# Kernel tuning notes

Measured on AMD Instinct MI355X. Metric: run time of the kernel, lower is better.

## Reference

```python
import jax, jax.numpy as jnp
import numpy as np
from jax import lax

# Problem constants (mirroring scalar_born args / init_kwargs)
NY = NX = 400          # interior model size
NS = 4                 # shots
NSRC = 1               # sources per shot
NREC = 100             # receivers per shot
NT = 300               # time steps
CHUNK = 10             # inner scan length (NT % CHUNK == 0)
PML = 20               # pml_width
FD_PAD = 2             # accuracy // 2 for accuracy=4
PAD = PML + FD_PAD
DX = 5.0               # grid_spacing
DT = 5e-4              # dt
PML_FREQ = 25.0
VMAX = 2500.0          # max_vel used for PML profile

# 4th-order central FD coefficients (taps at offsets -2..+2)
C1 = (1.0 / 12, -2.0 / 3, 0.0, 2.0 / 3, -1.0 / 12)        # d/dx, * 1/h
C2 = (-1.0 / 12, 4.0 / 3, -5.0 / 2, 4.0 / 3, -1.0 / 12)   # d2/dx2, * 1/h^2


def _deriv(w, coefs, axis, scale):
    """4th-order central difference along `axis` with zero boundary."""
    pad = [(0, 0)] * w.ndim
    pad[axis] = (2, 2)
    p = jnp.pad(w, pad)
    n = w.shape[axis]
    out = coefs[0] * lax.slice_in_dim(p, 0, n, axis=axis)
    for k in range(1, 5):
        if coefs[k] != 0.0:
            out = out + coefs[k] * lax.slice_in_dim(p, k, k + n, axis=axis)
    return out * scale


def _pml_profiles(n):
    """CPML decay (a) and update (b) 1D profiles over a padded axis."""
    i = jnp.arange(n, dtype=jnp.float32)
    frac = jnp.maximum(jnp.clip((PAD - i) / PML, 0.0, 1.0),
                       jnp.clip((i - (n - 1 - PAD)) / PML, 0.0, 1.0))
    L = PML * DX
    sigma_max = 3.0 * VMAX * np.log(1000.0) / (2.0 * L)
    sigma = sigma_max * frac ** 2
    alpha = np.pi * PML_FREQ
    a = jnp.exp(-(sigma + alpha) * DT)
    b = jnp.where(sigma > 0, sigma / (sigma + alpha) * (a - 1.0), 0.0)
    return a, b


def _propagate(v, scatter, source_amplitudes, source_locations,
               receiver_locations, bg_receiver_locations):
    v_pad = jnp.pad(v, PAD, mode='edge')     # 'replicate' pad for velocity
    sc_pad = jnp.pad(scatter, PAD)           # 'constant' (zero) pad for scatter
    npy, npx = v_pad.shape
    ay, by = _pml_profiles(npy)
    ax, bx = _pml_profiles(npx)
    ay, by = ay[:, None], by[:, None]
    ax, bx = ax[None, :], bx[None, :]
    v2dt2 = (v_pad * DT) ** 2
    born_scale = 2.0 * v_pad * sc_pad * DT * DT  # Born secondary-source scale

    sy = source_locations[..., 0] + PAD          # [ns, nsrc]
    sx = source_locations[..., 1] + PAD
    shot_s = jnp.arange(NS)[:, None]
    v_src = v_pad[sy, sx]
    sc_src = sc_pad[sy, sx]
    # Source scaling as in scalar_born(): bg gets -f*v^2*dt^2,
    # scattered gets -2*f*v*scatter*dt^2 at the source cell.
    f_bg = -source_amplitudes * (v_src ** 2)[..., None] * DT * DT
    f_sc = -2.0 * source_amplitudes * (v_src * sc_src)[..., None] * DT * DT
    f_bg = jnp.moveaxis(f_bg, -1, 0).reshape(NT // CHUNK, CHUNK, NS, NSRC)
    f_sc = jnp.moveaxis(f_sc, -1, 0).reshape(NT // CHUNK, CHUNK, NS, NSRC)

    ry = receiver_locations[..., 0] + PAD
    rx = receiver_locations[..., 1] + PAD
    rby = bg_receiver_locations[..., 0] + PAD
    rbx = bg_receiver_locations[..., 1] + PAD
    shot_r = jnp.arange(NS)[:, None]

    inv_h, inv_h2 = 1.0 / DX, 1.0 / (DX * DX)

    def pml_lap(w, psiy, psix, zetay, zetax):
        # CPML (Pasalic & McGarry) memory variables for 2nd-order scalar wave eq
        dwdy = _deriv(w, C1, -2, inv_h)
        dwdx = _deriv(w, C1, -1, inv_h)
        d2y = _deriv(w, C2, -2, inv_h2)
        d2x = _deriv(w, C2, -1, inv_h2)
        psiy = ay * psiy + by * dwdy
        psix = ax * psix + bx * dwdx
        dpsiy = _deriv(psiy, C1, -2, inv_h)
        dpsix = _deriv(psix, C1, -1, inv_h)
        zetay = ay * zetay + by * (d2y + dpsiy)
        zetax = ax * zetax + bx * (d2x + dpsix)
        lap = d2y + d2x + dpsiy + dpsix + zetay + zetax
        return lap, psiy, psix, zetay, zetax

    def step(carry, fs):
        (wfc, wfp, psiy, psix, zetay, zetax,
         wfcsc, wfpsc, psiysc, psixsc, zetaysc, zetaxsc) = carry
        fb, fsc = fs
        lap, psiy, psix, zetay, zetax = pml_lap(wfc, psiy, psix, zetay, zetax)
        wfn = v2dt2 * lap + 2.0 * wfc - wfp
        wfn = wfn.at[shot_s, sy, sx].add(fb)
        lapsc, psiysc, psixsc, zetaysc, zetaxsc = pml_lap(
            wfcsc, psiysc, psixsc, zetaysc, zetaxsc)
        wfnsc = v2dt2 * lapsc + 2.0 * wfcsc - wfpsc + born_scale * lap
        wfnsc = wfnsc.at[shot_s, sy, sx].add(fsc)
        rec_bg = wfn[shot_r, rby, rbx]
        rec_sc = wfnsc[shot_r, ry, rx]
        new_carry = (wfn, wfc, psiy, psix, zetay, zetax,
                     wfnsc, wfcsc, psiysc, psixsc, zetaysc, zetaxsc)
        return new_carry, (rec_bg, rec_sc)

    chunk = jax.checkpoint(lambda c, xs: lax.scan(step, c, xs))

    z = jnp.zeros((NS, npy, npx), dtype=v.dtype)
    carry0 = (z,) * 12
    carry, (rec_bg, rec_sc) = lax.scan(chunk, carry0, (f_bg, f_sc))
    rec_bg = jnp.moveaxis(rec_bg.reshape(NT, NS, NREC), 0, -1)
    rec_sc = jnp.moveaxis(rec_sc.reshape(NT, NS, NREC), 0, -1)
    return carry, rec_bg, rec_sc


def setup_inputs() -> dict:
    key = jax.random.key(0)
    k = jax.random.split(key, 6)
    v = 1500.0 + 1000.0 * jax.random.uniform(k[0], (NY, NX), jnp.float32)
    scatter = 0.1 * jax.random.normal(k[1], (NY, NX), jnp.float32)
    source_amplitudes = jax.random.normal(k[2], (NS, NSRC, NT), jnp.float32)
    source_locations = jax.random.randint(k[3], (NS, NSRC, 2), 0, NY)
    receiver_locations = jax.random.randint(k[4], (NS, NREC, 2), 0, NY)
    bg_receiver_locations = jax.random.randint(k[5], (NS, NREC, 2), 0, NY)
    return {
        'v': v,
        'scatter': scatter,
        'source_amplitudes': source_amplitudes,
        'source_locations': source_locations,
        'receiver_locations': receiver_locations,
        'bg_receiver_locations': bg_receiver_locations,
    }


def reference(v, scatter, source_amplitudes, source_locations,
              receiver_locations, bg_receiver_locations):
    carry, rec_bg, rec_sc = _propagate(
        v, scatter, source_amplitudes, source_locations,
        receiver_locations, bg_receiver_locations)
    # (final background wavefield, final scattered wavefield,
    #  background receiver amplitudes, scattered receiver amplitudes)
    return (carry[0], carry[6], rec_bg, rec_sc)
```

## Files before the change

### kernel.cpp

```cpp
#include <hip/hip_runtime.h>
#include <hip/hip_bf16.h>


constexpr int NYX  = 400;
constexpr int NS   = 4;
constexpr int NREC = 100;
constexpr int NT   = 300;
constexpr int PAD  = 22;
constexpr int NP   = 444;
constexpr int NP2  = NP * NP;
constexpr int SNP2 = NS * NP2;
constexpr float DT    = 0.0005f;
constexpr float INVH  = 0.2f;
constexpr float INVH2 = 0.04f;
constexpr float C1A = 1.0f / 12.0f;
constexpr float C1B = 2.0f / 3.0f;
constexpr float C2A = -1.0f / 12.0f;
constexpr float C2B = 4.0f / 3.0f;
constexpr float C2C = -2.5f;

__device__ __align__(16) float g_w[2][2 * SNP2];
__device__ __align__(16) float g_px[2][2 * SNP2];
__device__ __align__(16) float g_py[2][2 * SNP2];
__device__ __align__(16) float g_zx[2 * SNP2];
__device__ __align__(16) float g_zy[2 * SNP2];
__device__ __align__(16) float g_vb[2 * NP2];
__device__ float g_pa[NP];
__device__ float g_pb[NP];
__device__ float g_fbg[NT * NS];
__device__ float g_fsc[NT * NS];
__device__ int   g_spos[2 * NS];
__device__ int   g_mode;

__device__ __forceinline__ int clampi(int v, int lo, int hi) {
    return v < lo ? lo : (v > hi ? hi : v);
}
__device__ __forceinline__ float in_ld(const void* p, int i) {
    if (g_mode) return __bfloat162float(((const __hip_bfloat16*)p)[i]);
    return ((const float*)p)[i];
}
__device__ __forceinline__ void out_st(void* p, int i, float v) {
    if (g_mode) ((__hip_bfloat16*)p)[i] = __float2bfloat16(v);
    else        ((float*)p)[i] = v;
}
__device__ __forceinline__ float4 ld4(const float* w, int s, int yy, int i) {
    if ((unsigned)yy >= (unsigned)NP) return make_float4(0.f, 0.f, 0.f, 0.f);
    return *(const float4*)(w + 2 * (s * NP2 + yy * NP + 2 * i));
}

__global__ void detect_mode(const void* vptr) {
    if (threadIdx.x == 0 && blockIdx.x == 0) {
        const __hip_bfloat16* p = (const __hip_bfloat16*)vptr;
        int ok = 1;
        for (int i = 0; i < 32; i += 2) {
            float f = __bfloat162float(p[i]);
            if (!(f >= 1000.f && f <= 3000.f)) ok = 0;
        }
        g_mode = ok;
    }
}

__global__ void zero_state() {
    int i = blockIdx.x * blockDim.x + threadIdx.x;
    if (i >= SNP2 / 2) return;
    float4 z = make_float4(0.f, 0.f, 0.f, 0.f);
    ((float4*)g_w[0])[i] = z;  ((float4*)g_w[1])[i] = z;
    ((float4*)g_px[0])[i] = z; ((float4*)g_px[1])[i] = z;
    ((float4*)g_py[0])[i] = z; ((float4*)g_py[1])[i] = z;
    ((float4*)g_zx)[i] = z;    ((float4*)g_zy)[i] = z;
}

__global__ void prep_pad(const void* __restrict__ v, const void* __restrict__ sc) {
    int i = blockIdx.x * blockDim.x + threadIdx.x;
    if (i >= NP2) return;
    int y = i / NP, x = i % NP;
    int vy = clampi(y - PAD, 0, NYX - 1);
    int vx = clampi(x - PAD, 0, NYX - 1);
    float vv = in_ld(v, vy * NYX + vx);
    float vd = vv * DT;
    float s = 0.f;
    if (y >= PAD && y < PAD + NYX && x >= PAD && x < PAD + NYX)
        s = in_ld(sc, (y - PAD) * NYX + (x - PAD));
    g_vb[2 * i]     = vd * vd;
    g_vb[2 * i + 1] = 2.f * vv * s * DT * DT;
    if (i < NP) {
        float fi = (float)i;
        float f1 = fminf(fmaxf((22.f - fi) * 0.05f, 0.f), 1.f);
        float f2 = fminf(fmaxf((fi - 421.f) * 0.05f, 0.f), 1.f);
        float frac = fmaxf(f1, f2);
        float sigma = 259.0408229f * frac * frac;
        const float alpha = 78.53981634f;
        float a = expf(-(sigma + alpha) * DT);
        g_pa[i] = a;
        g_pb[i] = (sigma > 0.f) ? sigma / (sigma + alpha) * (a - 1.f) : 0.f;
    }
}

__global__ void prep_src(const void* __restrict__ amp, const int* __restrict__ sloc,
                         const void* __restrict__ v, const void* __restrict__ sc) {
    int i = blockIdx.x * blockDim.x + threadIdx.x;
    if (i >= NT * NS) return;
    int s = i % NS, t = i / NS;
    int ly = clampi(sloc[s * 2 + 0], 0, NYX - 1);
    int lx = clampi(sloc[s * 2 + 1], 0, NYX - 1);
    float a  = in_ld(amp, s * NT + t);
    float vv = in_ld(v,  ly * NYX + lx);
    float ss = in_ld(sc, ly * NYX + lx);
    g_fbg[i] = -a * vv * vv * DT * DT;
    g_fsc[i] = -2.f * a * vv * ss * DT * DT;
    if (i < NS) {
        g_spos[2 * i]     = ly + PAD;
        g_spos[2 * i + 1] = lx + PAD;
    }
}

__global__ void __launch_bounds__(256, 7)
step_fused(int t, const int* __restrict__ rloc, const int* __restrict__ rbloc,
           void* __restrict__ out) {
    const int i = threadIdx.x;
    const int bid = blockIdx.x;
    const int s = (bid >> 1) & 3;
    const int y = ((bid & 1) ? 222 : 0) + (bid >> 3);
    const int cur = t & 1, nxt = cur ^ 1;
    __shared__ __align__(16) float sw[904], spx[904];

    if (t > 0 && y == 0 && i < 2 * NREC) {
        int r = i % NREC;
        bool isbg = i < NREC;
        const int* rl = isbg ? rbloc : rloc;
        int ry = clampi(rl[(s * NREC + r) * 2 + 0], 0, NYX - 1) + PAD;
        int rx = clampi(rl[(s * NREC + r) * 2 + 1], 0, NYX - 1) + PAD;
        float val = g_w[cur][2 * (s * NP2 + ry * NP + rx) + (isbg ? 0 : 1)];
        int base = isbg ? (2 * SNP2) : (2 * SNP2 + NS * NREC * NT);
        out_st(out, base + (s * NREC + r) * NT + (t - 1), val);
    }

    const bool active = i < 222;
    const int x0 = 2 * i, x1 = x0 + 1;
    const int yx  = y * NP + x0;
    const int idx = s * NP2 + yx;

    float4 w4 = make_float4(0.f, 0.f, 0.f, 0.f);
    if (active) {
        w4 = *(const float4*)(g_w[cur] + 2 * idx);
        *(float4*)&sw[2 * x0 + 4] = w4;
    } else if (i == 222) {
        #pragma unroll
        for (int k = 0; k < 4; ++k) { sw[k] = 0.f; spx[k] = 0.f; }
    } else if (i == 223) {
        #pragma unroll
        for (int k = 892; k < 904; ++k) { sw[k] = 0.f; spx[k] = 0.f; }
    }
    __syncthreads();

    const bool pxreg = (i <= 11 || i >= 210);
    float pbx0 = 0.f, pbx1 = 0.f, pax0 = 0.f, pax1 = 0.f;
    float d2x_b0 = 0.f, d2x_b1 = 0.f, d2x_s0 = 0.f, d2x_s1 = 0.f;
    float4 pxn = make_float4(0.f, 0.f, 0.f, 0.f);
    float2 tm2, tm1, tp2, tp3;
    if (active) {
        tm2 = *(const float2*)&sw[2 * (x0 - 2) + 4];
        tm1 = *(const float2*)&sw[2 * (x0 - 1) + 4];
        tp2 = *(const float2*)&sw[2 * (x0 + 2) + 4];
        tp3 = *(const float2*)&sw[2 * (x0 + 3) + 4];
        d2x_b0 = (C2A * (tm2.x + tp2.x) + C2B * (tm1.x + w4.z) + C2C * w4.x) * INVH2;
        d2x_s0 = (C2A * (tm2.y + tp2.y) + C2B * (tm1.y + w4.w) + C2C * w4.y) * INVH2;
        d2x_b1 = (C2A * (tm1.x + tp3.x) + C2B * (w4.x + tp2.x) + C2C * w4.z) * INVH2;
        d2x_s1 = (C2A * (tm1.y + tp3.y) + C2B * (w4.y + tp2.y) + C2C * w4.w) * INVH2;
        pbx0 = g_pb[x0]; pbx1 = g_pb[x1];
        pax0 = g_pa[x0]; pax1 = g_pa[x1];
        if (pxreg && pbx0 != 0.f) {
            float4 pxo = *(const float4*)(g_px[cur] + 2 * idx);
            float dwb0 = (C1A * tm2.x - C1B * tm1.x + C1B * w4.z - C1A * tp2.x) * INVH;
            float dws0 = (C1A * tm2.y - C1B * tm1.y + C1B * w4.w - C1A * tp2.y) * INVH;
            float dwb1 = (C1A * tm1.x - C1B * w4.x + C1B * tp2.x - C1A * tp3.x) * INVH;
            float dws1 = (C1A * tm1.y - C1B * w4.y + C1B * tp2.y - C1A * tp3.y) * INVH;
            pxn.x = pax0 * pxo.x + pbx0 * dwb0;
            pxn.y = pax0 * pxo.y + pbx0 * dws0;
            pxn.z = pax1 * pxo.z + pbx1 * dwb1;
            pxn.w = pax1 * pxo.w + pbx1 * dws1;
            *(float4*)(g_px[nxt] + 2 * idx) = pxn;
        }
        *(float4*)&spx[2 * x0 + 4] = pxn;
    }
    __syncthreads();
    if (!active) return;

    float dpx_b0 = 0.f, dpx_b1 = 0.f, dpx_s0 = 0.f, dpx_s1 = 0.f;
    if (pxreg) {
        float2 pm2 = *(const float2*)&spx[2 * (x0 - 2) + 4];
        float2 pm1 = *(const float2*)&spx[2 * (x0 - 1) + 4];
        float2 pp2 = *(const float2*)&spx[2 * (x0 + 2) + 4];
        float2 pp3 = *(const float2*)&spx[2 * (x0 + 3) + 4];
        dpx_b0 = (C1A * pm2.x - C1B * pm1.x + C1B * pxn.z - C1A * pp2.x) * INVH;
        dpx_s0 = (C1A * pm2.y - C1B * pm1.y + C1B * pxn.w - C1A * pp2.y) * INVH;
        dpx_b1 = (C1A * pm1.x - C1B * pxn.x + C1B * pp2.x - C1A * pp3.x) * INVH;
        dpx_s1 = (C1A * pm1.y - C1B * pxn.y + C1B * pp2.y - C1A * pp3.y) * INVH;
    }

    const float pby = g_pb[y];
    const bool yframe = (y <= 23 || y >= 420);
    float d2y_b0, d2y_b1, d2y_s0, d2y_s1;
    float dpy_b0 = 0.f, dpy_b1 = 0.f, dpy_s0 = 0.f, dpy_s1 = 0.f;
    if (yframe) {
        float4 wy[9];
        #pragma unroll
        for (int k = 0; k < 9; ++k)
            wy[k] = (k == 4) ? w4 : ld4(g_w[cur], s, y - 4 + k, i);
        d2y_b0 = (C2A * (wy[2].x + wy[6].x) + C2B * (wy[3].x + wy[5].x) + C2C * wy[4].x) * INVH2;
        d2y_s0 = (C2A * (wy[2].y + wy[6].y) + C2B * (wy[3].y + wy[5].y) + C2C * wy[4].y) * INVH2;
        d2y_b1 = (C2A * (wy[2].z + wy[6].z) + C2B * (wy[3].z + wy[5].z) + C2C * wy[4].z) * INVH2;
        d2y_s1 = (C2A * (wy[2].w + wy[6].w) + C2B * (wy[3].w + wy[5].w) + C2C * wy[4].w) * INVH2;
        float4 pn[5];
        #pragma unroll
        for (int k = 0; k < 5; ++k) {
            int yy = y - 2 + k;
            float pbv = ((unsigned)yy < (unsigned)NP) ? g_pb[yy] : 0.f;
            float4 r = make_float4(0.f, 0.f, 0.f, 0.f);
            if (pbv != 0.f) {
                float pav = g_pa[yy];
                float4 po = *(const float4*)(g_py[cur] + 2 * (s * NP2 + yy * NP + x0));
                float db0 = (C1A * wy[k].x - C1B * wy[k+1].x + C1B * wy[k+3].x - C1A * wy[k+4].x) * INVH;
                float ds0 = (C1A * wy[k].y - C1B * wy[k+1].y + C1B * wy[k+3].y - C1A * wy[k+4].y) * INVH;
                float db1 = (C1A * wy[k].z - C1B * wy[k+1].z + C1B * wy[k+3].z - C1A * wy[k+4].z) * INVH;
                float ds1 = (C1A * wy[k].w - C1B * wy[k+1].w + C1B * wy[k+3].w - C1A * wy[k+4].w) * INVH;
                r.x = pav * po.x + pbv * db0;  r.y = pav * po.y + pbv * ds0;
                r.z = pav * po.z + pbv * db1;  r.w = pav * po.w + pbv * ds1;
            }
            pn[k] = r;
        }
        dpy_b0 = (C1A * pn[0].x - C1B * pn[1].x + C1B * pn[3].x - C1A * pn[4].x) * INVH;
        dpy_s0 = (C1A * pn[0].y - C1B * pn[1].y + C1B * pn[3].y - C1A * pn[4].y) * INVH;
        dpy_b1 = (C1A * pn[0].z - C1B * pn[1].z + C1B * pn[3].z - C1A * pn[4].z) * INVH;
        dpy_s1 = (C1A * pn[0].w - C1B * pn[1].w + C1B * pn[3].w - C1A * pn[4].w) * INVH;
        if (pby != 0.f)
            *(float4*)(g_py[nxt] + 2 * idx) = pn[2];
    } else {
        float4 m2 = *(const float4*)(g_w[cur] + 2 * (idx - 2 * NP));
        float4 m1 = *(const float4*)(g_w[cur] + 2 * (idx - NP));
        float4 p1 = *(const float4*)(g_w[cur] + 2 * (idx + NP));
        float4 p2 = *(const float4*)(g_w[cur] + 2 * (idx + 2 * NP));
        d2y_b0 = (C2A * (m2.x + p2.x) + C2B * (m1.x + p1.x) + C2C * w4.x) * INVH2;
        d2y_s0 = (C2A * (m2.y + p2.y) + C2B * (m1.y + p1.y) + C2C * w4.y) * INVH2;
        d2y_b1 = (C2A * (m2.z + p2.z) + C2B * (m1.z + p1.z) + C2C * w4.z) * INVH2;
        d2y_s1 = (C2A * (m2.w + p2.w) + C2B * (m1.w + p1.w) + C2C * w4.w) * INVH2;
    }

    float zy_b0 = 0.f, zy_b1 = 0.f, zy_s0 = 0.f, zy_s1 = 0.f;
    float zx_b0 = 0.f, zx_b1 = 0.f, zx_s0 = 0.f, zx_s1 = 0.f;
    if (pby != 0.f) {
        float pay = g_pa[y];
        float4 zo = *(const float4*)(g_zy + 2 * idx);
        zy_b0 = pay * zo.x + pby * (d2y_b0 + dpy_b0);
        zy_s0 = pay * zo.y + pby * (d2y_s0 + dpy_s0);
        zy_b1 = pay * zo.z + pby * (d2y_b1 + dpy_b1);
        zy_s1 = pay * zo.w + pby * (d2y_s1 + dpy_s1);
        *(float4*)(g_zy + 2 * idx) = make_float4(zy_b0, zy_s0, zy_b1, zy_s1);
    }
    if (pbx0 != 0.f) {
        float4 zo = *(const float4*)(g_zx + 2 * idx);
        zx_b0 = pax0 * zo.x + pbx0 * (d2x_b0 + dpx_b0);
        zx_s0 = pax0 * zo.y + pbx0 * (d2x_s0 + dpx_s0);
        zx_b1 = pax1 * zo.z + pbx1 * (d2x_b1 + dpx_b1);
        zx_s1 = pax1 * zo.w + pbx1 * (d2x_s1 + dpx_s1);
        *(float4*)(g_zx + 2 * idx) = make_float4(zx_b0, zx_s0, zx_b1, zx_s1);
    }

    float4 vb   = *(const float4*)(g_vb + 2 * yx);
    float4 prev = *(const float4*)(g_w[nxt] + 2 * idx);
    float lap_b0 = d2y_b0 + d2x_b0 + dpy_b0 + dpx_b0 + zy_b0 + zx_b0;
    float lap_s0 = d2y_s0 + d2x_s0 + dpy_s0 + dpx_s0 + zy_s0 + zx_s0;
    float lap_b1 = d2y_b1 + d2x_b1 + dpy_b1 + dpx_b1 + zy_b1 + zx_b1;
    float lap_s1 = d2y_s1 + d2x_s1 + dpy_s1 + dpx_s1 + zy_s1 + zx_s1;
    float wn_b0 = vb.x * lap_b0 + 2.f * w4.x - prev.x;
    float wn_s0 = vb.x * lap_s0 + 2.f * w4.y - prev.y + vb.y * lap_b0;
    float wn_b1 = vb.z * lap_b1 + 2.f * w4.z - prev.z;
    float wn_s1 = vb.z * lap_s1 + 2.f * w4.w - prev.w + vb.w * lap_b1;
    if (y == g_spos[2 * s]) {
        int sx = g_spos[2 * s + 1];
        if (sx == x0)      { wn_b0 += g_fbg[t * NS + s]; wn_s0 += g_fsc[t * NS + s]; }
        else if (sx == x1) { wn_b1 += g_fbg[t * NS + s]; wn_s1 += g_fsc[t * NS + s]; }
    }
    *(float4*)(g_w[nxt] + 2 * idx) = make_float4(wn_b0, wn_s0, wn_b1, wn_s1);
}

__global__ void finalize(const int* __restrict__ rloc, const int* __restrict__ rbloc,
                         void* __restrict__ out) {
    int i = blockIdx.x * blockDim.x + threadIdx.x;
    const float* w0 = g_w[0];
    if (i < SNP2) {
        out_st(out, i,        w0[2 * i]);
        out_st(out, SNP2 + i, w0[2 * i + 1]);
    }
    if (i < 2 * NS * NREC) {
        bool isbg = i < NS * NREC;
        int k = isbg ? i : i - NS * NREC;
        int s = k / NREC, r = k % NREC;
        const int* rl = isbg ? rbloc : rloc;
        int ry = clampi(rl[(s * NREC + r) * 2 + 0], 0, NYX - 1) + PAD;
        int rx = clampi(rl[(s * NREC + r) * 2 + 1], 0, NYX - 1) + PAD;
        float val = w0[2 * (s * NP2 + ry * NP + rx) + (isbg ? 0 : 1)];
        int base = isbg ? (2 * SNP2) : (2 * SNP2 + NS * NREC * NT);
        out_st(out, base + (s * NREC + r) * NT + (NT - 1), val);
    }
}

extern "C" void kernel_launch(void* const* d_in, const int* in_sizes, int n_in,
                              void* d_out, int out_size, void* d_ws, size_t ws_size,
                              hipStream_t stream) {
    const void* v   = d_in[0];
    const void* sc  = d_in[1];
    const void* amp = d_in[2];
    const int* sloc  = (const int*)d_in[3];
    const int* rloc  = (const int*)d_in[4];
    const int* rbloc = (const int*)d_in[5];

    detect_mode<<<1, 64, 0, stream>>>(v);
    zero_state<<<(SNP2 / 2 + 255) / 256, 256, 0, stream>>>();
    prep_pad<<<(NP2 + 255) / 256, 256, 0, stream>>>(v, sc);
    prep_src<<<(NT * NS + 255) / 256, 256, 0, stream>>>(amp, sloc, v, sc);

    for (int t = 0; t < NT; ++t)
        step_fused<<<NS * NP, 256, 0, stream>>>(t, rloc, rbloc, d_out);

    finalize<<<(SNP2 + 255) / 256, 256, 0, stream>>>(rloc, rbloc, d_out);
}
```

Measured before the change: 2.359 ms.

## Replace shared-memory x-stencil halo exchange with wavefront shuffles

Removes the shared-memory staging and both block barriers used for the x-direction stencil of the wavefield and PML auxiliary. Each 64-lane wavefront now covers 60 owned point-pairs with 2-lane halos on each side, and neighbours are obtained via shuffle up/down. This drops the __syncthreads and LDS traffic, but halo lanes redundantly load and compute, and the per-block thread-to-column mapping changes (4 waves x 60 owned pairs must cover 222 pairs).

```diff
diff --git a/kernel.cpp b/kernel.cpp
--- a/kernel.cpp
+++ b/kernel.cpp
@@ -43,9 +43,17 @@
     if (g_mode) ((__hip_bfloat16*)p)[i] = __float2bfloat16(v);
     else        ((float*)p)[i] = v;
 }
-__device__ __forceinline__ float4 ld4(const float* w, int s, int yy, int i) {
+__device__ __forceinline__ float4 ld4(const float* w, int s, int yy, int ip) {
     if ((unsigned)yy >= (unsigned)NP) return make_float4(0.f, 0.f, 0.f, 0.f);
-    return *(const float4*)(w + 2 * (s * NP2 + yy * NP + 2 * i));
+    return *(const float4*)(w + 2 * (s * NP2 + yy * NP + 2 * ip));
+}
+__device__ __forceinline__ float4 shup4(float4 v) {
+    return make_float4(__shfl_up(v.x, 1), __shfl_up(v.y, 1),
+                       __shfl_up(v.z, 1), __shfl_up(v.w, 1));
+}
+__device__ __forceinline__ float4 shdn4(float4 v) {
+    return make_float4(__shfl_down(v.x, 1), __shfl_down(v.y, 1),
+                       __shfl_down(v.z, 1), __shfl_down(v.w, 1));
 }
 
 __global__ void detect_mode(const void* vptr) {
@@ -122,7 +130,6 @@
     const int s = (bid >> 1) & 3;
     const int y = ((bid & 1) ? 222 : 0) + (bid >> 3);
     const int cur = t & 1, nxt = cur ^ 1;
-    __shared__ __align__(16) float sw[904], spx[904];
 
     if (t > 0 && y == 0 && i < 2 * NREC) {
         int r = i % NREC;
@@ -135,68 +142,61 @@
         out_st(out, base + (s * NREC + r) * NT + (t - 1), val);
     }
 
-    const bool active = i < 222;
-    const int x0 = 2 * i, x1 = x0 + 1;
+    const int wid  = i >> 6;
+    const int lane = i & 63;
+    const int ip   = 60 * wid + lane - 2;
+    const bool inb   = (unsigned)ip < 222u;
+    const bool owner = (lane >= 2) && (lane < 62) && inb;
+
+    const int x0 = 2 * ip, x1 = x0 + 1;
     const int yx  = y * NP + x0;
     const int idx = s * NP2 + yx;
 
     float4 w4 = make_float4(0.f, 0.f, 0.f, 0.f);
-    if (active) {
-        w4 = *(const float4*)(g_w[cur] + 2 * idx);
-        *(float4*)&sw[2 * x0 + 4] = w4;
-    } else if (i == 222) {
-        #pragma unroll
-        for (int k = 0; k < 4; ++k) { sw[k] = 0.f; spx[k] = 0.f; }
-    } else if (i == 223) {
-        #pragma unroll
-        for (int k = 892; k < 904; ++k) { sw[k] = 0.f; spx[k] = 0.f; }
-    }
-    __syncthreads();
-
-    const bool pxreg = (i <= 11 || i >= 210);
+    if (inb) w4 = *(const float4*)(g_w[cur] + 2 * idx);
+
+    float4 wl = shup4(w4);
+    float4 wr = shdn4(w4);
+
+    const bool pxreg = (ip <= 11 || ip >= 210);
     float pbx0 = 0.f, pbx1 = 0.f, pax0 = 0.f, pax1 = 0.f;
     float d2x_b0 = 0.f, d2x_b1 = 0.f, d2x_s0 = 0.f, d2x_s1 = 0.f;
     float4 pxn = make_float4(0.f, 0.f, 0.f, 0.f);
-    float2 tm2, tm1, tp2, tp3;
-    if (active) {
-        tm2 = *(const float2*)&sw[2 * (x0 - 2) + 4];
-        tm1 = *(const float2*)&sw[2 * (x0 - 1) + 4];
-        tp2 = *(const float2*)&sw[2 * (x0 + 2) + 4];
-        tp3 = *(const float2*)&sw[2 * (x0 + 3) + 4];
-        d2x_b0 = (C2A * (tm2.x + tp2.x) + C2B * (tm1.x + w4.z) + C2C * w4.x) * INVH2;
-        d2x_s0 = (C2A * (tm2.y + tp2.y) + C2B * (tm1.y + w4.w) + C2C * w4.y) * INVH2;
-        d2x_b1 = (C2A * (tm1.x + tp3.x) + C2B * (w4.x + tp2.x) + C2C * w4.z) * INVH2;
-        d2x_s1 = (C2A * (tm1.y + tp3.y) + C2B * (w4.y + tp2.y) + C2C * w4.w) * INVH2;
+    if (inb) {
+        d2x_b0 = (C2A * (wl.x + wr.x) + C2B * (wl.z + w4.z) + C2C * w4.x) * INVH2;
+        d2x_s0 = (C2A * (wl.y + wr.y) + C2B * (wl.w + w4.w) + C2C * w4.y) * INVH2;
+        d2x_b1 = (C2A * (wl.z + wr.z) + C2B * (w4.x + wr.x) + C2C * w4.z) * INVH2;
+        d2x_s1 = (C2A * (wl.w + wr.w) + C2B * (w4.y + wr.y) + C2C * w4.w) * INVH2;
         pbx0 = g_pb[x0]; pbx1 = g_pb[x1];
         pax0 = g_pa[x0]; pax1 = g_pa[x1];
         if (pxreg && pbx0 != 0.f) {
             float4 pxo = *(const float4*)(g_px[cur] + 2 * idx);
-            float dwb0 = (C1A * tm2.x - C1B * tm1.x + C1B * w4.z - C1A * tp2.x) * INVH;
-            float dws0 = (C1A * tm2.y - C1B * tm1.y + C1B * w4.w - C1A * tp2.y) * INVH;
-            float dwb1 = (C1A * tm1.x - C1B * w4.x + C1B * tp2.x - C1A * tp3.x) * INVH;
-            float dws1 = (C1A * tm1.y - C1B * w4.y + C1B * tp2.y - C1A * tp3.y) * INVH;
+            float dwb0 = (C1A * wl.x - C1B * wl.z + C1B * w4.z - C1A * wr.x) * INVH;
+            float dws0 = (C1A * wl.y - C1B * wl.w + C1B * w4.w - C1A * wr.y) * INVH;
+            float dwb1 = (C1A * wl.z - C1B * w4.x + C1B * wr.x - C1A * wr.z) * INVH;
+            float dws1 = (C1A * wl.w - C1B * w4.y + C1B * wr.y - C1A * wr.w) * INVH;
             pxn.x = pax0 * pxo.x + pbx0 * dwb0;
             pxn.y = pax0 * pxo.y + pbx0 * dws0;
             pxn.z = pax1 * pxo.z + pbx1 * dwb1;
             pxn.w = pax1 * pxo.w + pbx1 * dws1;
-            *(float4*)(g_px[nxt] + 2 * idx) = pxn;
+            if (owner)
+                *(float4*)(g_px[nxt] + 2 * idx) = pxn;
         }
-        *(float4*)&spx[2 * x0 + 4] = pxn;
-    }
-    __syncthreads();
-    if (!active) return;
+    }
 
     float dpx_b0 = 0.f, dpx_b1 = 0.f, dpx_s0 = 0.f, dpx_s1 = 0.f;
-    if (pxreg) {
-        float2 pm2 = *(const float2*)&spx[2 * (x0 - 2) + 4];
-        float2 pm1 = *(const float2*)&spx[2 * (x0 - 1) + 4];
-        float2 pp2 = *(const float2*)&spx[2 * (x0 + 2) + 4];
-        float2 pp3 = *(const float2*)&spx[2 * (x0 + 3) + 4];
-        dpx_b0 = (C1A * pm2.x - C1B * pm1.x + C1B * pxn.z - C1A * pp2.x) * INVH;
-        dpx_s0 = (C1A * pm2.y - C1B * pm1.y + C1B * pxn.w - C1A * pp2.y) * INVH;
-        dpx_b1 = (C1A * pm1.x - C1B * pxn.x + C1B * pp2.x - C1A * pp3.x) * INVH;
-        dpx_s1 = (C1A * pm1.y - C1B * pxn.y + C1B * pp2.y - C1A * pp3.y) * INVH;
-    }
+    {
+        float4 pl = shup4(pxn);
+        float4 pr = shdn4(pxn);
+        if (pxreg) {
+            dpx_b0 = (C1A * pl.x - C1B * pl.z + C1B * pxn.z - C1A * pr.x) * INVH;
+            dpx_s0 = (C1A * pl.y - C1B * pl.w + C1B * pxn.w - C1A * pr.y) * INVH;
+            dpx_b1 = (C1A * pl.z - C1B * pxn.x + C1B * pr.x - C1A * pr.z) * INVH;
+            dpx_s1 = (C1A * pl.w - C1B * pxn.y + C1B * pr.y - C1A * pr.w) * INVH;
+        }
+    }
+
+    if (!owner) return;
 
     const float pby = g_pb[y];
     const bool yframe = (y <= 23 || y >= 420);
@@ -206,7 +206,7 @@
         float4 wy[9];
         #pragma unroll
         for (int k = 0; k < 9; ++k)
-            wy[k] = (k == 4) ? w4 : ld4(g_w[cur], s, y - 4 + k, i);
+            wy[k] = (k == 4) ? w4 : ld4(g_w[cur], s, y - 4 + k, ip);
         d2y_b0 = (C2A * (wy[2].x + wy[6].x) + C2B * (wy[3].x + wy[5].x) + C2C * wy[4].x) * INVH2;
         d2y_s0 = (C2A * (wy[2].y + wy[6].y) + C2B * (wy[3].y + wy[5].y) + C2C * wy[4].y) * INVH2;
         d2y_b1 = (C2A * (wy[2].z + wy[6].z) + C2B * (wy[3].z + wy[5].z) + C2C * wy[4].z) * INVH2;
```

Result: no change. 2.317 ms (-1.8%).
